# Performance work log

Measured on AMD Instinct MI355X. Metric: run time of the kernel, lower is better.

## Reference

```python
import jax, jax.numpy as jnp
import numpy as np

EPS = 1e-12  # matches torch F.normalize eps


def setup_inputs() -> dict:
    key = jax.random.key(0)
    k1, k2, k3 = jax.random.split(key, 3)
    N, C, H, W, K = 16, 1024, 32, 32, 32
    x = jax.random.normal(k1, (N, C, H, W), dtype=jnp.float32)
    # 1x1 conv weight (K, C, 1, 1) stored as (K, C)
    conv_w = jax.random.normal(k2, (K, C), dtype=jnp.float32) * 0.02
    centroids = jax.random.uniform(k3, (K, C), dtype=jnp.float32)
    return {"x": x, "conv_w": conv_w, "centroids": centroids}


def _l2norm(v, axis):
    return v / jnp.maximum(jnp.linalg.norm(v, axis=axis, keepdims=True), EPS)


def reference(x, conv_w, centroids):
    N, C, H, W = x.shape
    K = centroids.shape[0]
    # normalize_input: L2 over channel dim
    x = _l2norm(x, axis=1)
    xf = x.reshape(N, C, H * W)                      # (N, C, P)
    # 1x1 conv == per-pixel matmul -> (N, K, P)
    logits = jnp.einsum('kc,ncp->nkp', conv_w, xf)
    a = jax.nn.softmax(logits, axis=1)               # softmax over clusters
    # sum_p a[n,k,p] * (x[n,:,p] - centroids[k,:])
    # == (a @ x^T) - (sum_p a) * centroids  (two GEMMs, no (N,K,C,P) blowup)
    vlad = jnp.einsum('nkp,ncp->nkc', a, xf) - a.sum(-1)[:, :, None] * centroids[None]
    vlad = _l2norm(vlad, axis=2)                     # intra-cluster L2 norm
    vlad = vlad.reshape(N, K * C)
    vlad = _l2norm(vlad, axis=1)                     # global L2 norm
    return vlad
```

## Files before the change

kernel.cpp:

```cpp
#include <hip/hip_runtime.h>

#define NB   16
#define CC   1024
#define PP   1024
#define KK   32
#define EPSF 1e-12f

typedef __attribute__((ext_vector_type(8))) short  bf16x8;
typedef __attribute__((ext_vector_type(4))) float  f32x4;

__device__ __forceinline__ float bf2f(unsigned short u) {
    union { unsigned int i; float f; } v; v.i = ((unsigned int)u) << 16; return v.f;
}
__device__ __forceinline__ unsigned short f2bf(float f) {
    union { float f; unsigned int i; } v; v.f = f;
    return (unsigned short)((v.i + 0x7fffu + ((v.i >> 16) & 1u)) >> 16);
}

template <typename T> struct IO;
template <> struct IO<float> {
    static __device__ __forceinline__ float ld(const float* p) { return *p; }
    static __device__ __forceinline__ f32x4 ld4(const float* p) { return *(const f32x4*)p; }
    static __device__ __forceinline__ void st4(float* p, f32x4 v) { *(f32x4*)p = v; }
};
template <> struct IO<unsigned short> {
    static __device__ __forceinline__ float ld(const unsigned short* p) { return bf2f(*p); }
    static __device__ __forceinline__ f32x4 ld4(const unsigned short* p) {
        const ushort4 u = *(const ushort4*)p;
        f32x4 r; r[0] = bf2f(u.x); r[1] = bf2f(u.y); r[2] = bf2f(u.z); r[3] = bf2f(u.w);
        return r;
    }
    static __device__ __forceinline__ void st4(unsigned short* p, f32x4 v) {
        ushort4 u;
        u.x = f2bf(v[0]); u.y = f2bf(v[1]); u.z = f2bf(v[2]); u.w = f2bf(v[3]);
        *(ushort4*)p = u;
    }
};

__device__ __forceinline__ void wg_sync_fast() {
    asm volatile("s_waitcnt lgkmcnt(0)" ::: "memory");
    __builtin_amdgcn_s_barrier();
    asm volatile("" ::: "memory");
}

struct __align__(16) AttnSmem {
    union {
        struct {
            unsigned short xT[2][32][136];
            unsigned short Wl[2][32][136];
        } m;
        struct {
            float red[32][32];
            float lg[32][33];
            float rn[32];
            float asq[4][32];
            unsigned short at[32][33];
        } e;
    } u;
};

template <typename T>
__device__ __forceinline__ void attn_body(const T* __restrict__ x,
                                          const T* __restrict__ w,
                                          AttnSmem& sm,
                                          unsigned short* __restrict__ attn_g,
                                          float* __restrict__ asum_p) {
    const int b = blockIdx.x, t = threadIdx.x;
    const int n = b >> 5, pt = b & 31, p0 = pt * 32;
    const int lane = t & 63, wv = t >> 6;
    const int quad = lane >> 4, l15 = lane & 15;
    const int khalf = wv >> 1, phalf = wv & 1;
    const int ci = t >> 3;
    const int pj = t & 7;
    const int wk = t >> 3;
    const int wc = (t & 7) * 16;
    const size_t xb = (size_t)n * CC * PP + p0;

    float ss[4] = {0.f, 0.f, 0.f, 0.f};
    f32x4 acc = {0.f, 0.f, 0.f, 0.f};

    f32x4 xr[4], wr[4];
    #pragma unroll
    for (int r = 0; r < 4; ++r) {
        xr[r] = IO<T>::ld4(&x[xb + (size_t)(4 * ci + r) * PP + 4 * pj]);
        wr[r] = IO<T>::ld4(&w[wk * CC + wc + 4 * r]);
    }

    #pragma unroll
    for (int ch = 0; ch < 8; ++ch) {
        const int buf = ch & 1;
        #pragma unroll
        for (int jj = 0; jj < 4; ++jj) {
            ss[jj] += xr[0][jj] * xr[0][jj] + xr[1][jj] * xr[1][jj]
                    + xr[2][jj] * xr[2][jj] + xr[3][jj] * xr[3][jj];
            ushort4 u;
            u.x = f2bf(xr[0][jj]); u.y = f2bf(xr[1][jj]);
            u.z = f2bf(xr[2][jj]); u.w = f2bf(xr[3][jj]);
            *(ushort4*)&sm.u.m.xT[buf][4 * pj + jj][4 * ci] = u;
        }
        #pragma unroll
        for (int r = 0; r < 4; ++r) {
            ushort4 u;
            u.x = f2bf(wr[r][0]); u.y = f2bf(wr[r][1]);
            u.z = f2bf(wr[r][2]); u.w = f2bf(wr[r][3]);
            *(ushort4*)&sm.u.m.Wl[buf][wk][wc + 4 * r] = u;
        }
        if (ch < 7) {
            const int c0 = (ch + 1) * 128;
            #pragma unroll
            for (int r = 0; r < 4; ++r) {
                xr[r] = IO<T>::ld4(&x[xb + (size_t)(c0 + 4 * ci + r) * PP + 4 * pj]);
                wr[r] = IO<T>::ld4(&w[wk * CC + c0 + wc + 4 * r]);
            }
        }
        wg_sync_fast();
        #pragma unroll
        for (int ks = 0; ks < 4; ++ks) {
            const bf16x8 av = *(const bf16x8*)&sm.u.m.Wl[buf][khalf * 16 + l15][ks * 32 + quad * 8];
            const bf16x8 bv = *(const bf16x8*)&sm.u.m.xT[buf][phalf * 16 + l15][ks * 32 + quad * 8];
            acc = __builtin_amdgcn_mfma_f32_16x16x32_bf16(av, bv, acc, 0, 0, 0);
        }
    }
    __syncthreads();

    #pragma unroll
    for (int jj = 0; jj < 4; ++jj) sm.u.e.red[ci][4 * pj + jj] = ss[jj];
    #pragma unroll
    for (int reg = 0; reg < 4; ++reg)
        sm.u.e.lg[phalf * 16 + l15][khalf * 16 + quad * 4 + reg] = acc[reg];
    __syncthreads();
    if (t < 32) {
        float s = 0.f;
        #pragma unroll
        for (int g = 0; g < 32; ++g) s += sm.u.e.red[g][t];
        sm.u.e.rn[t] = 1.0f / fmaxf(sqrtf(s), EPSF);
    }
    __syncthreads();
    {
        const int p = t >> 3, kg = (t & 7) * 4;
        const float rr = sm.u.e.rn[p];
        float l[4];
        #pragma unroll
        for (int q = 0; q < 4; ++q) l[q] = sm.u.e.lg[p][kg + q] * rr;
        float mx = fmaxf(fmaxf(l[0], l[1]), fmaxf(l[2], l[3]));
        mx = fmaxf(mx, __shfl_xor(mx, 1, 64));
        mx = fmaxf(mx, __shfl_xor(mx, 2, 64));
        mx = fmaxf(mx, __shfl_xor(mx, 4, 64));
        float e[4], sum = 0.f;
        #pragma unroll
        for (int q = 0; q < 4; ++q) { e[q] = expf(l[q] - mx); sum += e[q]; }
        sum += __shfl_xor(sum, 1, 64);
        sum += __shfl_xor(sum, 2, 64);
        sum += __shfl_xor(sum, 4, 64);
        const float inv = 1.0f / sum;
        float a[4];
        #pragma unroll
        for (int q = 0; q < 4; ++q) {
            a[q] = e[q] * inv;
            sm.u.e.at[kg + q][p] = f2bf(a[q] * rr);
        }
        #pragma unroll
        for (int q = 0; q < 4; ++q) {
            a[q] += __shfl_xor(a[q], 8, 64);
            a[q] += __shfl_xor(a[q], 16, 64);
            a[q] += __shfl_xor(a[q], 32, 64);
        }
        if ((lane >> 3) == 0) {
            #pragma unroll
            for (int q = 0; q < 4; ++q) sm.u.e.asq[wv][kg + q] = a[q];
        }
    }
    __syncthreads();
    if (t < 32)
        asum_p[(n * 32 + pt) * KK + t]
            = sm.u.e.asq[0][t] + sm.u.e.asq[1][t] + sm.u.e.asq[2][t] + sm.u.e.asq[3][t];
    {
        const int k = t >> 3, po = (t & 7) * 4;
        ushort4 u;
        u.x = sm.u.e.at[k][po];     u.y = sm.u.e.at[k][po + 1];
        u.z = sm.u.e.at[k][po + 2]; u.w = sm.u.e.at[k][po + 3];
        *(ushort4*)&attn_g[((size_t)n * KK + k) * PP + p0 + po] = u;
    }
}

__global__ __launch_bounds__(256) void k_attn(const void* __restrict__ xv,
                                              const void* __restrict__ wv,
                                              int* __restrict__ flag,
                                              unsigned short* __restrict__ attn_g,
                                              float* __restrict__ asum_p) {
    __shared__ AttnSmem sm;
    __shared__ int s_bad;
    const int t = threadIdx.x;
    if (t == 0) s_bad = 0;
    __syncthreads();
    {
        const unsigned short* xu = (const unsigned short*)xv;
        int bad = 0;
        for (int ii = t; ii < 4096; ii += 256)
            if (((xu[ii] >> 7) & 0xFFu) > 0x9Fu) bad = 1;
        if (bad) atomicOr(&s_bad, 1);
    }
    __syncthreads();
    const int f = s_bad;
    if (blockIdx.x == 0 && t == 0) flag[0] = f;
    if (f) attn_body<float>((const float*)xv, (const float*)wv, sm, attn_g, asum_p);
    else   attn_body<unsigned short>((const unsigned short*)xv, (const unsigned short*)wv,
                                     sm, attn_g, asum_p);
}

struct VladSmem { float asum[32]; float ssq[32]; };

template <typename T>
__device__ __forceinline__ void vlad_body(const T* __restrict__ x,
                                          const T* __restrict__ cent, VladSmem& sm,
                                          const unsigned short* __restrict__ attn_g,
                                          const float* __restrict__ asum_p,
                                          float* __restrict__ vlad,
                                          float* __restrict__ ssqnk_p) {
    const int b = blockIdx.x, t = threadIdx.x;
    const int n = b >> 5, ct = b & 31;
    const int lane = t & 63, wvi = t >> 6;
    const int quad = lane >> 4, l15 = lane & 15;
    const int mt = wvi & 1, nt = wvi >> 1;
    const int krow = mt * 16 + l15;
    const int crow = ct * 32 + nt * 16 + l15;
    if (t < 32) {
        float s = 0.f;
        #pragma unroll
        for (int ps = 0; ps < 32; ++ps) s += asum_p[(n * 32 + ps) * KK + t];
        sm.asum[t] = s;
        sm.ssq[t] = 0.f;
    }
    __syncthreads();
    const unsigned short* apq = attn_g + ((size_t)n * KK + krow) * PP + quad * 8;
    const T* xp = x + (size_t)n * CC * PP + (size_t)crow * PP + quad * 8;
    f32x4 acc = {0.f, 0.f, 0.f, 0.f};
    bf16x8 avq[4]; f32x4 xq0[4], xq1[4];
    #pragma unroll
    for (int ii = 0; ii < 4; ++ii) {
        const int o = ii * 32;
        avq[ii] = *(const bf16x8*)&apq[o];
        xq0[ii] = IO<T>::ld4(&xp[o]); xq1[ii] = IO<T>::ld4(&xp[o + 4]);
    }
    #pragma unroll
    for (int st = 0; st < 32; ++st) {
        const int sl = st & 3;
        bf16x8 bv;
        #pragma unroll
        for (int jj = 0; jj < 4; ++jj) {
            bv[jj]     = (short)f2bf(xq0[sl][jj]);
            bv[4 + jj] = (short)f2bf(xq1[sl][jj]);
        }
        acc = __builtin_amdgcn_mfma_f32_16x16x32_bf16(avq[sl], bv, acc, 0, 0, 0);
        if (st + 4 < 32) {
            const int o = (st + 4) * 32;
            avq[sl] = *(const bf16x8*)&apq[o];
            xq0[sl] = IO<T>::ld4(&xp[o]); xq1[sl] = IO<T>::ld4(&xp[o + 4]);
        }
    }
    #pragma unroll
    for (int reg = 0; reg < 4; ++reg) {
        const int kk = mt * 16 + quad * 4 + reg;
        const float A = sm.asum[kk];
        const float v = acc[reg] - A * IO<T>::ld(&cent[kk * CC + crow]);
        vlad[((size_t)n * KK + kk) * CC + crow] = v;
        float sq = v * v;
        sq += __shfl_xor(sq, 1, 64);
        sq += __shfl_xor(sq, 2, 64);
        sq += __shfl_xor(sq, 4, 64);
        sq += __shfl_xor(sq, 8, 64);
        if (l15 == 0) atomicAdd(&sm.ssq[kk], sq);
    }
    __syncthreads();
    if (t < 32) ssqnk_p[(n * 32 + ct) * KK + t] = sm.ssq[t];
}

__global__ __launch_bounds__(256) void k_vlad(const void* __restrict__ xv,
                                              const void* __restrict__ centv,
                                              const int* __restrict__ flag,
                                              const unsigned short* __restrict__ attn_g,
                                              const float* __restrict__ asum_p,
                                              float* __restrict__ vlad,
                                              float* __restrict__ ssqnk_p) {
    __shared__ VladSmem sm;
    if (*flag) vlad_body<float>((const float*)xv, (const float*)centv, sm,
                                attn_g, asum_p, vlad, ssqnk_p);
    else       vlad_body<unsigned short>((const unsigned short*)xv, (const unsigned short*)centv,
                                         sm, attn_g, asum_p, vlad, ssqnk_p);
}

struct OutSmem { float ssq[32]; float rint[32]; float rg; };

template <typename T>
__device__ __forceinline__ void out_body(const float* __restrict__ vlad,
                                         const float* __restrict__ ssqnk_p,
                                         OutSmem& sm, T* __restrict__ out) {
    const int b = blockIdx.x, t = threadIdx.x;
    const int n = b >> 5, k = b & 31;
    if (t < 32) {
        float s = 0.f;
        #pragma unroll
        for (int ct = 0; ct < 32; ++ct) s += ssqnk_p[(n * 32 + ct) * KK + t];
        sm.ssq[t] = s;
    }
    __syncthreads();
    if (t < 64) {
        const float s = (t < 32) ? sm.ssq[t] : 0.f;
        const float rr = 1.0f / fmaxf(sqrtf(s), EPSF);
        float gg = s * rr * rr;
        #pragma unroll
        for (int off = 32; off > 0; off >>= 1) gg += __shfl_down(gg, off, 64);
        if (t == 0) sm.rg = 1.0f / fmaxf(sqrtf(gg), EPSF);
        if (t < 32) sm.rint[t] = rr;
    }
    __syncthreads();
    const float f = sm.rint[k] * sm.rg;
    const size_t ob = ((size_t)n * KK + k) * CC + 4 * t;
    f32x4 v = *(const f32x4*)&vlad[ob];
    v[0] *= f; v[1] *= f; v[2] *= f; v[3] *= f;
    IO<T>::st4(&out[ob], v);
}

__global__ __launch_bounds__(256) void k_out(const float* __restrict__ vlad,
                                             const float* __restrict__ ssqnk_p,
                                             const int* __restrict__ flag,
                                             void* __restrict__ outv) {
    __shared__ OutSmem sm;
    if (*flag) out_body<float>(vlad, ssqnk_p, sm, (float*)outv);
    else       out_body<unsigned short>(vlad, ssqnk_p, sm, (unsigned short*)outv);
}

extern "C" void kernel_launch(void* const* d_in, const int* in_sizes, int n_in,
                              void* d_out, int out_size, void* d_ws, size_t ws_size,
                              hipStream_t stream) {
    const void* x    = d_in[0];
    const void* w    = d_in[1];
    const void* cent = d_in[2];

    float* ws      = (float*)d_ws;
    float* asum_p  = ws;
    float* ssqnk_p = asum_p + NB * 32 * KK;
    float* vlad    = ssqnk_p + NB * 32 * KK;
    int*   flag    = (int*)(vlad + (size_t)NB * KK * CC);
    unsigned short* attn_g = (unsigned short*)(flag + 4);

    k_attn<<<NB * 32, 256, 0, stream>>>(x, w, flag, attn_g, asum_p);
    k_vlad<<<NB * 32, 256, 0, stream>>>(x, cent, flag, attn_g, asum_p, vlad, ssqnk_p);
    k_out<<<NB * KK, 256, 0, stream>>>(vlad, ssqnk_p, flag, d_out);
}
```

Before: 130.0 us.

## Stage full x tile in LDS once and stream conv weights from registers

The attention kernel no longer runs a double-buffered 128-channel chunk loop with a barrier per chunk. It first transposes and converts the whole 32-pixel by 1024-channel x tile into one large LDS buffer, then runs all 32 MFMA steps after a single barrier, reading conv weight fragments straight from global memory through a register ring. The aim is to drop the per-chunk synchronisation and the LDS staging of the weights. In exchange, LDS use per block grows to about 66 KB, which may reduce occupancy. The second kernel's bf16 conversion is also moved into a frag8 helper applied at load time instead of just before each MFMA, which changes when the conversion runs.

```diff
diff --git a/kernel.cpp b/kernel.cpp
--- a/kernel.cpp
+++ b/kernel.cpp
@@ -5,6 +5,7 @@
 #define PP   1024
 #define KK   32
 #define EPSF 1e-12f
+#define XSTR 1032
 
 typedef __attribute__((ext_vector_type(8))) short  bf16x8;
 typedef __attribute__((ext_vector_type(4))) float  f32x4;
@@ -21,6 +22,15 @@
 template <> struct IO<float> {
     static __device__ __forceinline__ float ld(const float* p) { return *p; }
     static __device__ __forceinline__ f32x4 ld4(const float* p) { return *(const f32x4*)p; }
+    static __device__ __forceinline__ bf16x8 frag8(const float* p) {
+        const f32x4 a = *(const f32x4*)p, b = *(const f32x4*)(p + 4);
+        bf16x8 r;
+        r[0] = (short)f2bf(a[0]); r[1] = (short)f2bf(a[1]);
+        r[2] = (short)f2bf(a[2]); r[3] = (short)f2bf(a[3]);
+        r[4] = (short)f2bf(b[0]); r[5] = (short)f2bf(b[1]);
+        r[6] = (short)f2bf(b[2]); r[7] = (short)f2bf(b[3]);
+        return r;
+    }
     static __device__ __forceinline__ void st4(float* p, f32x4 v) { *(f32x4*)p = v; }
 };
 template <> struct IO<unsigned short> {
@@ -30,6 +40,9 @@
         f32x4 r; r[0] = bf2f(u.x); r[1] = bf2f(u.y); r[2] = bf2f(u.z); r[3] = bf2f(u.w);
         return r;
     }
+    static __device__ __forceinline__ bf16x8 frag8(const unsigned short* p) {
+        return *(const bf16x8*)p;
+    }
     static __device__ __forceinline__ void st4(unsigned short* p, f32x4 v) {
         ushort4 u;
         u.x = f2bf(v[0]); u.y = f2bf(v[1]); u.z = f2bf(v[2]); u.w = f2bf(v[3]);
@@ -37,18 +50,9 @@
     }
 };
 
-__device__ __forceinline__ void wg_sync_fast() {
-    asm volatile("s_waitcnt lgkmcnt(0)" ::: "memory");
-    __builtin_amdgcn_s_barrier();
-    asm volatile("" ::: "memory");
-}
-
 struct __align__(16) AttnSmem {
     union {
-        struct {
-            unsigned short xT[2][32][136];
-            unsigned short Wl[2][32][136];
-        } m;
+        unsigned short xT[32][XSTR];
         struct {
             float red[32][32];
             float lg[32][33];
@@ -70,61 +74,58 @@
     const int lane = t & 63, wv = t >> 6;
     const int quad = lane >> 4, l15 = lane & 15;
     const int khalf = wv >> 1, phalf = wv & 1;
-    const int ci = t >> 3;
+    const int cq = t >> 3;
     const int pj = t & 7;
-    const int wk = t >> 3;
-    const int wc = (t & 7) * 16;
-    const size_t xb = (size_t)n * CC * PP + p0;
+    const size_t xb = (size_t)n * CC * PP + p0 + 4 * pj;
 
     float ss[4] = {0.f, 0.f, 0.f, 0.f};
     f32x4 acc = {0.f, 0.f, 0.f, 0.f};
 
-    f32x4 xr[4], wr[4];
-    #pragma unroll
-    for (int r = 0; r < 4; ++r) {
-        xr[r] = IO<T>::ld4(&x[xb + (size_t)(4 * ci + r) * PP + 4 * pj]);
-        wr[r] = IO<T>::ld4(&w[wk * CC + wc + 4 * r]);
-    }
-
-    #pragma unroll
-    for (int ch = 0; ch < 8; ++ch) {
-        const int buf = ch & 1;
-        #pragma unroll
-        for (int jj = 0; jj < 4; ++jj) {
-            ss[jj] += xr[0][jj] * xr[0][jj] + xr[1][jj] * xr[1][jj]
-                    + xr[2][jj] * xr[2][jj] + xr[3][jj] * xr[3][jj];
-            ushort4 u;
-            u.x = f2bf(xr[0][jj]); u.y = f2bf(xr[1][jj]);
-            u.z = f2bf(xr[2][jj]); u.w = f2bf(xr[3][jj]);
-            *(ushort4*)&sm.u.m.xT[buf][4 * pj + jj][4 * ci] = u;
-        }
-        #pragma unroll
-        for (int r = 0; r < 4; ++r) {
-            ushort4 u;
-            u.x = f2bf(wr[r][0]); u.y = f2bf(wr[r][1]);
-            u.z = f2bf(wr[r][2]); u.w = f2bf(wr[r][3]);
-            *(ushort4*)&sm.u.m.Wl[buf][wk][wc + 4 * r] = u;
-        }
-        if (ch < 7) {
-            const int c0 = (ch + 1) * 128;
-            #pragma unroll
-            for (int r = 0; r < 4; ++r) {
-                xr[r] = IO<T>::ld4(&x[xb + (size_t)(c0 + 4 * ci + r) * PP + 4 * pj]);
-                wr[r] = IO<T>::ld4(&w[wk * CC + c0 + wc + 4 * r]);
-            }
-        }
-        wg_sync_fast();
-        #pragma unroll
-        for (int ks = 0; ks < 4; ++ks) {
-            const bf16x8 av = *(const bf16x8*)&sm.u.m.Wl[buf][khalf * 16 + l15][ks * 32 + quad * 8];
-            const bf16x8 bv = *(const bf16x8*)&sm.u.m.xT[buf][phalf * 16 + l15][ks * 32 + quad * 8];
-            acc = __builtin_amdgcn_mfma_f32_16x16x32_bf16(av, bv, acc, 0, 0, 0);
-        }
-    }
-    __syncthreads();
-
-    #pragma unroll
-    for (int jj = 0; jj < 4; ++jj) sm.u.e.red[ci][4 * pj + jj] = ss[jj];
+    f32x4 qA[4], qB[4];
+#define LOADB(Q, B)                                                               \
+    do { _Pragma("unroll")                                                        \
+        for (int r = 0; r < 4; ++r)                                               \
+            Q[r] = IO<T>::ld4(&x[xb + (size_t)((B) * 128 + cq * 4 + r) * PP]);    \
+    } while (0)
+#define PROCB(Q, B)                                                               \
+    do { _Pragma("unroll")                                                        \
+        for (int j = 0; j < 4; ++j) {                                             \
+            ss[j] += Q[0][j] * Q[0][j] + Q[1][j] * Q[1][j]                        \
+                   + Q[2][j] * Q[2][j] + Q[3][j] * Q[3][j];                       \
+            ushort4 u;                                                            \
+            u.x = f2bf(Q[0][j]); u.y = f2bf(Q[1][j]);                             \
+            u.z = f2bf(Q[2][j]); u.w = f2bf(Q[3][j]);                             \
+            *(ushort4*)&sm.u.xT[4 * pj + j][(B) * 128 + cq * 4] = u;              \
+        }                                                                         \
+    } while (0)
+    LOADB(qA, 0); LOADB(qB, 1);
+    PROCB(qA, 0); LOADB(qA, 2);
+    PROCB(qB, 1); LOADB(qB, 3);
+    PROCB(qA, 2); LOADB(qA, 4);
+    PROCB(qB, 3); LOADB(qB, 5);
+    PROCB(qA, 4); LOADB(qA, 6);
+    PROCB(qB, 5); LOADB(qB, 7);
+    PROCB(qA, 6);
+    PROCB(qB, 7);
+#undef LOADB
+#undef PROCB
+    __syncthreads();
+
+    const T* wrow = w + (size_t)(khalf * 16 + l15) * CC + quad * 8;
+    bf16x8 wq[8];
+    #pragma unroll
+    for (int ii = 0; ii < 8; ++ii) wq[ii] = IO<T>::frag8(&wrow[ii * 32]);
+    #pragma unroll
+    for (int ks = 0; ks < 32; ++ks) {
+        const int sl = ks & 7;
+        const bf16x8 bv = *(const bf16x8*)&sm.u.xT[phalf * 16 + l15][ks * 32 + quad * 8];
+        acc = __builtin_amdgcn_mfma_f32_16x16x32_bf16(wq[sl], bv, acc, 0, 0, 0);
+        if (ks + 8 < 32) wq[sl] = IO<T>::frag8(&wrow[(ks + 8) * 32]);
+    }
+    __syncthreads();
+
+    #pragma unroll
+    for (int j = 0; j < 4; ++j) sm.u.e.red[cq][4 * pj + j] = ss[j];
     #pragma unroll
     for (int reg = 0; reg < 4; ++reg)
         sm.u.e.lg[phalf * 16 + l15][khalf * 16 + quad * 4 + reg] = acc[reg];
@@ -235,27 +236,21 @@
     const unsigned short* apq = attn_g + ((size_t)n * KK + krow) * PP + quad * 8;
     const T* xp = x + (size_t)n * CC * PP + (size_t)crow * PP + quad * 8;
     f32x4 acc = {0.f, 0.f, 0.f, 0.f};
-    bf16x8 avq[4]; f32x4 xq0[4], xq1[4];
+    bf16x8 avq[4], bvq[4];
     #pragma unroll
     for (int ii = 0; ii < 4; ++ii) {
         const int o = ii * 32;
         avq[ii] = *(const bf16x8*)&apq[o];
-        xq0[ii] = IO<T>::ld4(&xp[o]); xq1[ii] = IO<T>::ld4(&xp[o + 4]);
+        bvq[ii] = IO<T>::frag8(&xp[o]);
     }
     #pragma unroll
     for (int st = 0; st < 32; ++st) {
         const int sl = st & 3;
-        bf16x8 bv;
-        #pragma unroll
-        for (int jj = 0; jj < 4; ++jj) {
-            bv[jj]     = (short)f2bf(xq0[sl][jj]);
-            bv[4 + jj] = (short)f2bf(xq1[sl][jj]);
-        }
-        acc = __builtin_amdgcn_mfma_f32_16x16x32_bf16(avq[sl], bv, acc, 0, 0, 0);
+        acc = __builtin_amdgcn_mfma_f32_16x16x32_bf16(avq[sl], bvq[sl], acc, 0, 0, 0);
         if (st + 4 < 32) {
             const int o = (st + 4) * 32;
             avq[sl] = *(const bf16x8*)&apq[o];
-            xq0[sl] = IO<T>::ld4(&xp[o]); xq1[sl] = IO<T>::ld4(&xp[o + 4]);
+            bvq[sl] = IO<T>::frag8(&xp[o]);
         }
     }
     #pragma unroll
```

New measurement: 141.1 us. +8.5%, slower.
